# Kernel tuning notes

Hardware: AMD Instinct MI355X
Metric: run time of the kernel (lower is better)

## Reference

```python
import jax, jax.numpy as jnp
import numpy as np

N_NODES = 50000
N_EDGES = 1200000
D_FEAT = 64
HIDDEN = 32


def setup_inputs() -> dict:
    key = jax.random.key(0)
    ks = jax.random.split(key, 9)
    x = jax.random.normal(ks[0], (N_NODES, D_FEAT), dtype=jnp.float32)
    edge_index = jax.random.randint(ks[1], (2, N_EDGES), 0, N_NODES, dtype=jnp.int64)
    u = jax.random.normal(ks[2], (N_NODES,), dtype=jnp.float32)
    d_in = 2 * D_FEAT
    # MLP: Linear(d_in,H) -> relu -> Linear(H,H) -> relu -> Linear(H,1)
    W1 = jax.random.normal(ks[3], (d_in, HIDDEN), dtype=jnp.float32) / np.sqrt(d_in)
    b1 = jnp.zeros((HIDDEN,), dtype=jnp.float32)
    W2 = jax.random.normal(ks[4], (HIDDEN, HIDDEN), dtype=jnp.float32) / np.sqrt(HIDDEN)
    b2 = jnp.zeros((HIDDEN,), dtype=jnp.float32)
    W3 = jax.random.normal(ks[5], (HIDDEN, 1), dtype=jnp.float32) / np.sqrt(HIDDEN)
    b3 = jnp.zeros((1,), dtype=jnp.float32)
    return {"x": x, "edge_index": edge_index, "u": u,
            "W1": W1, "b1": b1, "W2": W2, "b2": b2, "W3": W3, "b3": b3}


def reference(x, edge_index, u, W1, b1, W2, b2, W3, b3):
    row, col = edge_index[0], edge_index[1]
    # gather + concat: [E, 2*D]
    x_edge = jnp.concatenate([x[row], x[col]], axis=-1)
    # per-edge MLP -> scalar weight per edge
    h = jax.nn.relu(x_edge @ W1 + b1)
    h = jax.nn.relu(h @ W2 + b2)
    edge_weight = (h @ W3 + b3)[:, 0]  # [E]
    # spmm: f[i] = sum_{e: row[e]==i} w_e * u[col[e]]
    f = jax.ops.segment_sum(edge_weight * u[col], row, num_segments=x.shape[0])
    return f
```

## Files before the change

### kernel.cpp

```cpp
#include <hip/hip_runtime.h>

#define N_NODES 50000
#define N_EDGES 1200000
#define N_TILES (N_NODES / 16)
#define W1T_STRIDE 72
#define K1_BLOCKS 782

#define N_BUCKETS 196
#define BUCKET_CAP 7168
#define EDGES_PER_BLOCK 1920
#define KA_BLOCKS 625
#define KB_SPLIT 4

typedef __attribute__((ext_vector_type(8))) short short8;
typedef __attribute__((ext_vector_type(4))) float floatx4;

__device__ __forceinline__ unsigned short f32_to_bf16(float f) {
    unsigned int v = __float_as_uint(f);
    unsigned int r = v + 0x7FFFu + ((v >> 16) & 1u);
    return (unsigned short)(r >> 16);
}
__device__ __forceinline__ float bf16_to_f32(unsigned short s) {
    return __uint_as_float(((unsigned int)s) << 16);
}
__device__ __forceinline__ unsigned int pack_bf16x2(float lo, float hi) {
    return (unsigned int)f32_to_bf16(lo) | ((unsigned int)f32_to_bf16(hi) << 16);
}

__global__ __launch_bounds__(256) void precompute_P_mfma(
    const float* __restrict__ x, const float* __restrict__ W1,
    const float* __restrict__ b1,
    unsigned short* __restrict__ P1, unsigned short* __restrict__ P2,
    int* __restrict__ cursor, float* __restrict__ out)
{
    const int tid  = threadIdx.x;
    const int gtid = blockIdx.x * 256 + tid;

    if (gtid < N_BUCKETS) cursor[gtid] = 0;
    for (int i = gtid; i < N_NODES; i += K1_BLOCKS * 256)
        out[i] = 0.0f;

    __shared__ unsigned short W1t[64 * W1T_STRIDE];
    for (int e = tid; e < 128 * 32; e += 256) {
        const int kp = e >> 5, jp = e & 31;
        W1t[((kp < 64) ? jp : jp + 32) * W1T_STRIDE + (kp & 63)] =
            f32_to_bf16(W1[e]);
    }
    __syncthreads();

    const int lane = tid & 63;
    const int n = lane & 15;
    const int q = lane >> 4;

    const int tile = blockIdx.x * 4 + (tid >> 6);
    if (tile >= N_TILES) return;

    short8 bw[4][2];
    #pragma unroll
    for (int G = 0; G < 4; ++G)
        #pragma unroll
        for (int h = 0; h < 2; ++h)
            bw[G][h] = *(const short8*)
                &W1t[(n + 16 * G) * W1T_STRIDE + h * 32 + q * 8];
    const float bias0 = b1[n], bias1 = b1[n + 16];

    const int node = tile * 16 + n;
    const float4* xp  = (const float4*)(x + (size_t)node * 64 + q * 8);
    const float4 xa = xp[0], xb = xp[1];
    const float4* xp2 = (const float4*)(x + (size_t)node * 64 + 32 + q * 8);
    const float4 xc = xp2[0], xd = xp2[1];

    short8 a0, a1;
    a0[0] = (short)f32_to_bf16(xa.x); a0[1] = (short)f32_to_bf16(xa.y);
    a0[2] = (short)f32_to_bf16(xa.z); a0[3] = (short)f32_to_bf16(xa.w);
    a0[4] = (short)f32_to_bf16(xb.x); a0[5] = (short)f32_to_bf16(xb.y);
    a0[6] = (short)f32_to_bf16(xb.z); a0[7] = (short)f32_to_bf16(xb.w);
    a1[0] = (short)f32_to_bf16(xc.x); a1[1] = (short)f32_to_bf16(xc.y);
    a1[2] = (short)f32_to_bf16(xc.z); a1[3] = (short)f32_to_bf16(xc.w);
    a1[4] = (short)f32_to_bf16(xd.x); a1[5] = (short)f32_to_bf16(xd.y);
    a1[6] = (short)f32_to_bf16(xd.z); a1[7] = (short)f32_to_bf16(xd.w);

    floatx4 acc[4];
    #pragma unroll
    for (int G = 0; G < 4; ++G) {
        const float bi = (G == 0) ? bias0 : (G == 1) ? bias1 : 0.0f;
        acc[G] = (floatx4){bi, bi, bi, bi};
        acc[G] = __builtin_amdgcn_mfma_f32_16x16x32_bf16(a0, bw[G][0], acc[G], 0, 0, 0);
        acc[G] = __builtin_amdgcn_mfma_f32_16x16x32_bf16(a1, bw[G][1], acc[G], 0, 0, 0);
    }
    unsigned int* P1d = (unsigned int*)P1;
    unsigned int* P2d = (unsigned int*)P2;
    #pragma unroll
    for (int r = 0; r < 4; ++r) {
        const int nr = tile * 16 + q * 4 + r;
        P1d[(size_t)nr * 16 + n] = pack_bf16x2(acc[0][r], acc[1][r]);
        P2d[(size_t)nr * 16 + n] = pack_bf16x2(acc[2][r], acc[3][r]);
    }
}

__global__ __launch_bounds__(256) void edge_bin(
    const int* __restrict__ row, const int* __restrict__ col,
    unsigned int* __restrict__ buf, int* __restrict__ cursor)
{
    __shared__ unsigned short rankv[EDGES_PER_BLOCK];
    __shared__ int hist[N_BUCKETS];
    __shared__ int base[N_BUCKETS];

    const int tid = threadIdx.x;
    for (int b = tid; b < N_BUCKETS; b += 256) hist[b] = 0;
    __syncthreads();

    const int blockStart = blockIdx.x * EDGES_PER_BLOCK;

    for (int i = tid; i < EDGES_PER_BLOCK; i += 256) {
        const int r = row[blockStart + i];
        rankv[i] = (unsigned short)atomicAdd(&hist[r >> 8], 1);
    }
    __syncthreads();

    for (int b = tid; b < N_BUCKETS; b += 256)
        base[b] = atomicAdd(&cursor[b], hist[b]);
    __syncthreads();

    for (int i = tid; i < EDGES_PER_BLOCK; i += 256) {
        const int r = row[blockStart + i];
        const int c = col[blockStart + i];
        const int bin = r >> 8;
        buf[(size_t)bin * BUCKET_CAP + base[bin] + (int)rankv[i]] =
            ((unsigned int)(r & 255) << 24) | (unsigned int)c;
    }
}

__global__ __launch_bounds__(256) void bucket_mlp(
    const float* __restrict__ u,
    const float* __restrict__ W2, const float* __restrict__ b2,
    const float* __restrict__ W3, const float* __restrict__ b3,
    const unsigned short* __restrict__ P1, const unsigned short* __restrict__ P2,
    const unsigned int* __restrict__ buf, const int* __restrict__ cursor,
    float* __restrict__ out)
{
    __shared__ float accs[256];
    const int tid = threadIdx.x;
    accs[tid] = 0.0f;

    const int b = blockIdx.x >> 2;
    const int s = blockIdx.x & (KB_SPLIT - 1);

    const int lane = tid & 63;
    const int n = lane & 15;
    const int q = lane >> 4;
    const int wave = tid >> 6;

    short8 bf0, bf1;
    #pragma unroll
    for (int i = 0; i < 8; ++i) {
        const int F = q * 4 + (i >> 1) + 16 * (i & 1);
        bf0[i] = (short)f32_to_bf16(W2[F * 32 + n]);
        bf1[i] = (short)f32_to_bf16(W2[F * 32 + n + 16]);
    }
    const float w3n0 = W3[n], w3n1 = W3[n + 16];
    const float b2n0 = b2[n], b2n1 = b2[n + 16];
    const float bias3 = b3[0];

    __syncthreads();

    const int cnt = cursor[b];
    const unsigned int* bb = buf + (size_t)b * BUCKET_CAP;
    const unsigned short* P1b = P1 + (size_t)b * 256 * 32;
    const int nch = (cnt + 31) >> 5;

    #pragma unroll 1
    for (int ch = s * 4 + wave; ch < nch; ch += KB_SPLIT * 4) {
        const int base0 = ch * 32;

        int rl[2], cI[2];
        #pragma unroll
        for (int t = 0; t < 2; ++t) {
            int e = base0 + t * 16 + n;
            if (e >= cnt) e = cnt - 1;
            const unsigned int ent = bb[e];
            rl[t] = (int)(ent >> 24);
            cI[t] = (int)(ent & 0x1FFFFu);
        }
        int r2 = 0; float u2 = 0.0f;
        if (n < 8) {
            const int eloc = base0 + 16 * (n >> 2) + 4 * q + (n & 3);
            const unsigned int ent2 = bb[(eloc < cnt) ? eloc : 0];
            r2 = (int)(ent2 >> 24);
            u2 = (eloc < cnt) ? u[ent2 & 0x1FFFFu] : 0.0f;
        }
        short8 v1[2], v2[2];
        #pragma unroll
        for (int t = 0; t < 2; ++t) {
            v1[t] = *(const short8*)(P1b + (size_t)rl[t] * 32 + q * 8);
            v2[t] = *(const short8*)(P2 + (size_t)cI[t] * 32 + q * 8);
        }

        float tr[2][4];
        #pragma unroll
        for (int t = 0; t < 2; ++t) {
            short8 a;
            #pragma unroll
            for (int i = 0; i < 8; ++i) {
                const float f1 = bf16_to_f32((unsigned short)v1[t][i]);
                const float f2 = bf16_to_f32((unsigned short)v2[t][i]);
                a[i] = (short)f32_to_bf16(fmaxf(f1 + f2, 0.0f));
            }
            floatx4 d0 = {b2n0, b2n0, b2n0, b2n0};
            floatx4 d1 = {b2n1, b2n1, b2n1, b2n1};
            d0 = __builtin_amdgcn_mfma_f32_16x16x32_bf16(a, bf0, d0, 0, 0, 0);
            d1 = __builtin_amdgcn_mfma_f32_16x16x32_bf16(a, bf1, d1, 0, 0, 0);
            #pragma unroll
            for (int r = 0; r < 4; ++r)
                tr[t][r] = fmaxf(d0[r], 0.0f) * w3n0 + fmaxf(d1[r], 0.0f) * w3n1;
        }

        #pragma unroll
        for (int mask = 1; mask < 16; mask <<= 1) {
            #pragma unroll
            for (int t = 0; t < 2; ++t)
                #pragma unroll
                for (int r = 0; r < 4; ++r)
                    tr[t][r] += __shfl_xor(tr[t][r], mask, 64);
        }

        if (n < 8) {
            const float va0 = (n & 4) ? tr[1][0] : tr[0][0];
            const float va1 = (n & 4) ? tr[1][1] : tr[0][1];
            const float va2 = (n & 4) ? tr[1][2] : tr[0][2];
            const float va3 = (n & 4) ? tr[1][3] : tr[0][3];
            const float vb0 = (n & 2) ? va2 : va0;
            const float vb1 = (n & 2) ? va3 : va1;
            const float v   = (n & 1) ? vb1 : vb0;
            atomicAdd(&accs[r2], (v + bias3) * u2);
        }
    }

    __syncthreads();

    const int node = b * 256 + tid;
    if (node < N_NODES) {
        const float val = accs[tid];
        atomicAdd(out + node, val);
    }
}

extern "C" void kernel_launch(void* const* d_in, const int* in_sizes, int n_in,
                              void* d_out, int out_size, void* d_ws, size_t ws_size,
                              hipStream_t stream)
{
    const float* x    = (const float*)d_in[0];
    const int*   eidx = (const int*)  d_in[1];
    const float* u    = (const float*)d_in[2];
    const float* W1   = (const float*)d_in[3];
    const float* b1   = (const float*)d_in[4];
    const float* W2   = (const float*)d_in[5];
    const float* b2   = (const float*)d_in[6];
    const float* W3   = (const float*)d_in[7];
    const float* b3   = (const float*)d_in[8];

    const int* row = eidx;
    const int* col = eidx + N_EDGES;

    unsigned short* P1 = (unsigned short*)d_ws;
    unsigned short* P2 = (unsigned short*)((char*)d_ws + (size_t)N_NODES * 64);
    unsigned int*  buf = (unsigned int*)((char*)d_ws + (size_t)N_NODES * 128);
    int* cursor = (int*)((char*)d_ws + (size_t)N_NODES * 128
                         + (size_t)N_BUCKETS * BUCKET_CAP * 4);
    float* out = (float*)d_out;

    precompute_P_mfma<<<K1_BLOCKS, 256, 0, stream>>>(x, W1, b1, P1, P2, cursor, out);

    edge_bin<<<KA_BLOCKS, 256, 0, stream>>>(row, col, buf, cursor);

    bucket_mlp<<<N_BUCKETS * KB_SPLIT, 256, 0, stream>>>(
        u, W2, b2, W3, b3, P1, P2, buf, cursor, out);
}
```

Measured before the change: 138.5 us.

## Fuse node precompute and edge binning into one launch; widen bucket MLP blocks

Merges the per-node W1 projection kernel and the edge binning kernel into one launch, with block index choosing the role and shared memory overlaid through a union. The cursor reset moves out to a memset issued before the fused kernel. The bucket MLP kernel goes from 256 to 512 threads per block, so eight waves stride over the chunks of each bucket. The aim is to drop a launch boundary and let the two independent phases run at the same time, and to raise parallelism per bucket. The cost is an added memset launch and more shared-accumulator atomic contention per block.

```diff
diff --git a/kernel.cpp b/kernel.cpp
--- a/kernel.cpp
+++ b/kernel.cpp
@@ -10,6 +10,7 @@
 #define BUCKET_CAP 7168
 #define EDGES_PER_BLOCK 1920
 #define KA_BLOCKS 625
+#define D1_BLOCKS (K1_BLOCKS + KA_BLOCKS)
 #define KB_SPLIT 4
 
 typedef __attribute__((ext_vector_type(8))) short short8;
@@ -27,111 +28,113 @@
     return (unsigned int)f32_to_bf16(lo) | ((unsigned int)f32_to_bf16(hi) << 16);
 }
 
-__global__ __launch_bounds__(256) void precompute_P_mfma(
+__global__ __launch_bounds__(256) void fused_pre_bin(
     const float* __restrict__ x, const float* __restrict__ W1,
     const float* __restrict__ b1,
+    const int* __restrict__ row, const int* __restrict__ col,
     unsigned short* __restrict__ P1, unsigned short* __restrict__ P2,
-    int* __restrict__ cursor, float* __restrict__ out)
+    unsigned int* __restrict__ buf, int* __restrict__ cursor,
+    float* __restrict__ out)
 {
-    const int tid  = threadIdx.x;
-    const int gtid = blockIdx.x * 256 + tid;
-
-    if (gtid < N_BUCKETS) cursor[gtid] = 0;
-    for (int i = gtid; i < N_NODES; i += K1_BLOCKS * 256)
-        out[i] = 0.0f;
-
-    __shared__ unsigned short W1t[64 * W1T_STRIDE];
-    for (int e = tid; e < 128 * 32; e += 256) {
-        const int kp = e >> 5, jp = e & 31;
-        W1t[((kp < 64) ? jp : jp + 32) * W1T_STRIDE + (kp & 63)] =
-            f32_to_bf16(W1[e]);
-    }
-    __syncthreads();
-
-    const int lane = tid & 63;
-    const int n = lane & 15;
-    const int q = lane >> 4;
-
-    const int tile = blockIdx.x * 4 + (tid >> 6);
-    if (tile >= N_TILES) return;
-
-    short8 bw[4][2];
-    #pragma unroll
-    for (int G = 0; G < 4; ++G)
-        #pragma unroll
-        for (int h = 0; h < 2; ++h)
-            bw[G][h] = *(const short8*)
-                &W1t[(n + 16 * G) * W1T_STRIDE + h * 32 + q * 8];
-    const float bias0 = b1[n], bias1 = b1[n + 16];
-
-    const int node = tile * 16 + n;
-    const float4* xp  = (const float4*)(x + (size_t)node * 64 + q * 8);
-    const float4 xa = xp[0], xb = xp[1];
-    const float4* xp2 = (const float4*)(x + (size_t)node * 64 + 32 + q * 8);
-    const float4 xc = xp2[0], xd = xp2[1];
-
-    short8 a0, a1;
-    a0[0] = (short)f32_to_bf16(xa.x); a0[1] = (short)f32_to_bf16(xa.y);
-    a0[2] = (short)f32_to_bf16(xa.z); a0[3] = (short)f32_to_bf16(xa.w);
-    a0[4] = (short)f32_to_bf16(xb.x); a0[5] = (short)f32_to_bf16(xb.y);
-    a0[6] = (short)f32_to_bf16(xb.z); a0[7] = (short)f32_to_bf16(xb.w);
-    a1[0] = (short)f32_to_bf16(xc.x); a1[1] = (short)f32_to_bf16(xc.y);
-    a1[2] = (short)f32_to_bf16(xc.z); a1[3] = (short)f32_to_bf16(xc.w);
-    a1[4] = (short)f32_to_bf16(xd.x); a1[5] = (short)f32_to_bf16(xd.y);
-    a1[6] = (short)f32_to_bf16(xd.z); a1[7] = (short)f32_to_bf16(xd.w);
-
-    floatx4 acc[4];
-    #pragma unroll
-    for (int G = 0; G < 4; ++G) {
-        const float bi = (G == 0) ? bias0 : (G == 1) ? bias1 : 0.0f;
-        acc[G] = (floatx4){bi, bi, bi, bi};
-        acc[G] = __builtin_amdgcn_mfma_f32_16x16x32_bf16(a0, bw[G][0], acc[G], 0, 0, 0);
-        acc[G] = __builtin_amdgcn_mfma_f32_16x16x32_bf16(a1, bw[G][1], acc[G], 0, 0, 0);
-    }
-    unsigned int* P1d = (unsigned int*)P1;
-    unsigned int* P2d = (unsigned int*)P2;
-    #pragma unroll
-    for (int r = 0; r < 4; ++r) {
-        const int nr = tile * 16 + q * 4 + r;
-        P1d[(size_t)nr * 16 + n] = pack_bf16x2(acc[0][r], acc[1][r]);
-        P2d[(size_t)nr * 16 + n] = pack_bf16x2(acc[2][r], acc[3][r]);
-    }
-}
-
-__global__ __launch_bounds__(256) void edge_bin(
-    const int* __restrict__ row, const int* __restrict__ col,
-    unsigned int* __restrict__ buf, int* __restrict__ cursor)
-{
-    __shared__ unsigned short rankv[EDGES_PER_BLOCK];
-    __shared__ int hist[N_BUCKETS];
-    __shared__ int base[N_BUCKETS];
+    __shared__ union {
+        unsigned short W1t[64 * W1T_STRIDE];
+        struct {
+            unsigned short rankv[EDGES_PER_BLOCK];
+            int hist[N_BUCKETS];
+            int base[N_BUCKETS];
+        } bin;
+    } sh;
 
     const int tid = threadIdx.x;
-    for (int b = tid; b < N_BUCKETS; b += 256) hist[b] = 0;
-    __syncthreads();
-
-    const int blockStart = blockIdx.x * EDGES_PER_BLOCK;
-
-    for (int i = tid; i < EDGES_PER_BLOCK; i += 256) {
-        const int r = row[blockStart + i];
-        rankv[i] = (unsigned short)atomicAdd(&hist[r >> 8], 1);
-    }
-    __syncthreads();
-
-    for (int b = tid; b < N_BUCKETS; b += 256)
-        base[b] = atomicAdd(&cursor[b], hist[b]);
-    __syncthreads();
-
-    for (int i = tid; i < EDGES_PER_BLOCK; i += 256) {
-        const int r = row[blockStart + i];
-        const int c = col[blockStart + i];
-        const int bin = r >> 8;
-        buf[(size_t)bin * BUCKET_CAP + base[bin] + (int)rankv[i]] =
-            ((unsigned int)(r & 255) << 24) | (unsigned int)c;
-    }
-}
-
-__global__ __launch_bounds__(256) void bucket_mlp(
+    const int bid = blockIdx.x;
+
+    if (bid < K1_BLOCKS) {
+        const int gtid = bid * 256 + tid;
+        for (int i = gtid; i < N_NODES; i += K1_BLOCKS * 256)
+            out[i] = 0.0f;
+
+        for (int e = tid; e < 128 * 32; e += 256) {
+            const int kp = e >> 5, jp = e & 31;
+            sh.W1t[((kp < 64) ? jp : jp + 32) * W1T_STRIDE + (kp & 63)] =
+                f32_to_bf16(W1[e]);
+        }
+        __syncthreads();
+
+        const int lane = tid & 63;
+        const int n = lane & 15;
+        const int q = lane >> 4;
+
+        const int tile = bid * 4 + (tid >> 6);
+        if (tile >= N_TILES) return;
+
+        short8 bw[4][2];
+        #pragma unroll
+        for (int G = 0; G < 4; ++G)
+            #pragma unroll
+            for (int h = 0; h < 2; ++h)
+                bw[G][h] = *(const short8*)
+                    &sh.W1t[(n + 16 * G) * W1T_STRIDE + h * 32 + q * 8];
+        const float bias0 = b1[n], bias1 = b1[n + 16];
+
+        const int node = tile * 16 + n;
+        const float4* xp  = (const float4*)(x + (size_t)node * 64 + q * 8);
+        const float4 xa = xp[0], xb = xp[1];
+        const float4* xp2 = (const float4*)(x + (size_t)node * 64 + 32 + q * 8);
+        const float4 xc = xp2[0], xd = xp2[1];
+
+        short8 a0, a1;
+        a0[0] = (short)f32_to_bf16(xa.x); a0[1] = (short)f32_to_bf16(xa.y);
+        a0[2] = (short)f32_to_bf16(xa.z); a0[3] = (short)f32_to_bf16(xa.w);
+        a0[4] = (short)f32_to_bf16(xb.x); a0[5] = (short)f32_to_bf16(xb.y);
+        a0[6] = (short)f32_to_bf16(xb.z); a0[7] = (short)f32_to_bf16(xb.w);
+        a1[0] = (short)f32_to_bf16(xc.x); a1[1] = (short)f32_to_bf16(xc.y);
+        a1[2] = (short)f32_to_bf16(xc.z); a1[3] = (short)f32_to_bf16(xc.w);
+        a1[4] = (short)f32_to_bf16(xd.x); a1[5] = (short)f32_to_bf16(xd.y);
+        a1[6] = (short)f32_to_bf16(xd.z); a1[7] = (short)f32_to_bf16(xd.w);
+
+        floatx4 acc[4];
+        #pragma unroll
+        for (int G = 0; G < 4; ++G) {
+            const float bi = (G == 0) ? bias0 : (G == 1) ? bias1 : 0.0f;
+            acc[G] = (floatx4){bi, bi, bi, bi};
+            acc[G] = __builtin_amdgcn_mfma_f32_16x16x32_bf16(a0, bw[G][0], acc[G], 0, 0, 0);
+            acc[G] = __builtin_amdgcn_mfma_f32_16x16x32_bf16(a1, bw[G][1], acc[G], 0, 0, 0);
+        }
+        unsigned int* P1d = (unsigned int*)P1;
+        unsigned int* P2d = (unsigned int*)P2;
+        #pragma unroll
+        for (int r = 0; r < 4; ++r) {
+            const int nr = tile * 16 + q * 4 + r;
+            P1d[(size_t)nr * 16 + n] = pack_bf16x2(acc[0][r], acc[1][r]);
+            P2d[(size_t)nr * 16 + n] = pack_bf16x2(acc[2][r], acc[3][r]);
+        }
+    } else {
+        for (int b = tid; b < N_BUCKETS; b += 256) sh.bin.hist[b] = 0;
+        __syncthreads();
+
+        const int blockStart = (bid - K1_BLOCKS) * EDGES_PER_BLOCK;
+
+        for (int i = tid; i < EDGES_PER_BLOCK; i += 256) {
+            const int r = row[blockStart + i];
+            sh.bin.rankv[i] = (unsigned short)atomicAdd(&sh.bin.hist[r >> 8], 1);
+        }
+        __syncthreads();
+
+        for (int b = tid; b < N_BUCKETS; b += 256)
+            sh.bin.base[b] = atomicAdd(&cursor[b], sh.bin.hist[b]);
+        __syncthreads();
+
+        for (int i = tid; i < EDGES_PER_BLOCK; i += 256) {
+            const int r = row[blockStart + i];
+            const int c = col[blockStart + i];
+            const int bin = r >> 8;
+            buf[(size_t)bin * BUCKET_CAP + sh.bin.base[bin] + (int)sh.bin.rankv[i]] =
+                ((unsigned int)(r & 255) << 24) | (unsigned int)c;
+        }
+    }
+}
+
+__global__ __launch_bounds__(512) void bucket_mlp(
     const float* __restrict__ u,
     const float* __restrict__ W2, const float* __restrict__ b2,
     const float* __restrict__ W3, const float* __restrict__ b3,
@@ -141,7 +144,7 @@
 {
     __shared__ float accs[256];
     const int tid = threadIdx.x;
-    accs[tid] = 0.0f;
+    if (tid < 256) accs[tid] = 0.0f;
 
     const int b = blockIdx.x >> 2;
     const int s = blockIdx.x & (KB_SPLIT - 1);
@@ -170,7 +173,7 @@
     const int nch = (cnt + 31) >> 5;
 
     #pragma unroll 1
-    for (int ch = s * 4 + wave; ch < nch; ch += KB_SPLIT * 4) {
+    for (int ch = s * 8 + wave; ch < nch; ch += KB_SPLIT * 8) {
         const int base0 = ch * 32;
 
         int rl[2], cI[2];
@@ -238,10 +241,9 @@
 
     __syncthreads();
 
-    const int node = b * 256 + tid;
-    if (node < N_NODES) {
-        const float val = accs[tid];
-        atomicAdd(out + node, val);
+    if (tid < 256) {
+        const int node = b * 256 + tid;
+        if (node < N_NODES) atomicAdd(out + node, accs[tid]);
     }
 }
 
@@ -269,10 +271,11 @@
                          + (size_t)N_BUCKETS * BUCKET_CAP * 4);
     float* out = (float*)d_out;
 
-    precompute_P_mfma<<<K1_BLOCKS, 256, 0, stream>>>(x, W1, b1, P1, P2, cursor, out);
-
-    edge_bin<<<KA_BLOCKS, 256, 0, stream>>>(row, col, buf, cursor);
-
-    bucket_mlp<<<N_BUCKETS * KB_SPLIT, 256, 0, stream>>>(
+    hipMemsetAsync(cursor, 0, N_BUCKETS * sizeof(int), stream);
+
+    fused_pre_bin<<<D1_BLOCKS, 256, 0, stream>>>(
+        x, W1, b1, row, col, P1, P2, buf, cursor, out);
+
+    bucket_mlp<<<N_BUCKETS * KB_SPLIT, 512, 0, stream>>>(
         u, W2, b2, W3, b3, P1, P2, buf, cursor, out);
 }
```

Result: faster. 135.6 us (-2.1%).
